# Kernel tuning notes

Hardware: AMD Instinct MI355X
Metric: run time of the kernel (lower is better)

Reference implementation:

```python
import jax, jax.numpy as jnp
import numpy as np

B, T, H, V = 16, 128, 512, 50257


def setup_inputs() -> dict:
    key = jax.random.key(0)
    ks = jax.random.split(key, 6)
    s = 0.05  # init_scale
    return {
        "tokens": jax.random.randint(ks[0], (B, T), 0, V, dtype=jnp.int32),
        "labels": jax.random.randint(ks[1], (B, T), 0, V, dtype=jnp.int32),
        "embedding": jax.random.normal(ks[2], (V, H), jnp.float32) * s,
        "W1": jax.random.normal(ks[3], (2 * H, 4 * H), jnp.float32) * s,
        "b1": jnp.zeros((4 * H,), jnp.float32),
        "W2": jax.random.normal(ks[4], (2 * H, 4 * H), jnp.float32) * s,
        "b2": jnp.zeros((4 * H,), jnp.float32),
        "softmax_w": jax.random.normal(ks[5], (H, V), jnp.float32) * s,
        "softmax_b": jnp.zeros((V,), jnp.float32),
    }


def _lstm_cell(x, h, c, W, b):
    # TF LSTMCell gate order: i, j (candidate), f, o; forget_bias = 0.0
    z = jnp.concatenate([x, h], axis=-1) @ W + b  # [B, 4H]
    i, j, f, o = jnp.split(z, 4, axis=-1)
    c_new = c * jax.nn.sigmoid(f) + jax.nn.sigmoid(i) * jnp.tanh(j)
    h_new = jnp.tanh(c_new) * jax.nn.sigmoid(o)
    return h_new, c_new


def _forward(tokens, labels, embedding, W1, b1, W2, b2, softmax_w, softmax_b):
    x = embedding[tokens]                 # [B, T, H] embedding lookup
    xs = jnp.swapaxes(x, 0, 1)            # [T, B, H] time-major for scan
    zeros = jnp.zeros((B, H), x.dtype)

    def step(carry, xt):
        c1, h1, c2, h2 = carry
        h1n, c1n = _lstm_cell(xt, h1, c1, W1, b1)
        h2n, c2n = _lstm_cell(h1n, h2, c2, W2, b2)
        return (c1n, h1n, c2n, h2n), h2n

    _, hs = jax.lax.scan(step, (zeros, zeros, zeros, zeros), xs)  # hs: [T, B, H]
    output = jnp.swapaxes(hs, 0, 1).reshape(-1, H)                # [B*T, H]
    logits = output @ softmax_w + softmax_b                       # [B*T, V]
    logp = jax.nn.log_softmax(logits, axis=-1)
    ll = jnp.take_along_axis(logp, labels.reshape(-1, 1), axis=1)[:, 0]
    cost = -jnp.sum(ll) / B  # sequence_loss_by_example summed, / batch_size
    return cost


def reference(tokens, labels, embedding, W1, b1, W2, b2, softmax_w, softmax_b):
    return _forward(tokens, labels, embedding, W1, b1, W2, b2, softmax_w, softmax_b)
```

## Files before the change

kernel.cpp:

```cpp
#include <hip/hip_runtime.h>

#define B_ 16
#define T_ 128
#define H_ 512
#define V_ 50257
#define VP_ 50304
#define NBLK 393
#define M_ (B_*T_)
#define N4H 2048
#define KH 512
#define NKB 16
#define FP_ 32
#define NTILES (NBLK * 16)
#define NWORK 224
#define NCHUNK (VP_ * 16 / 16)
#define HP_ 520

typedef __attribute__((ext_vector_type(8))) short short8;
typedef __attribute__((ext_vector_type(4))) float floatx4;
typedef unsigned long long u64;

static __device__ __forceinline__ unsigned short f2bf(float f) {
    unsigned int u = __builtin_bit_cast(unsigned int, f);
    unsigned int r = (u + 0x7FFFu + ((u >> 16) & 1u)) >> 16;
    return (unsigned short)r;
}
static __device__ __forceinline__ u64 ld_ic(const u64* p) {
    return __hip_atomic_load(p, __ATOMIC_RELAXED, __HIP_MEMORY_SCOPE_AGENT);
}
static __device__ __forceinline__ void st_ic(u64* p, u64 v) {
    __hip_atomic_store(p, v, __ATOMIC_RELAXED, __HIP_MEMORY_SCOPE_AGENT);
}
static __device__ __forceinline__ short8 mk_frag(u64 a, u64 b) {
    union { u64 u[2]; short8 s8; } cv;
    cv.u[0] = a; cv.u[1] = b;
    return cv.s8;
}

__global__ void k_init(const int* __restrict__ labels, int* __restrict__ lab_r,
                       unsigned short* __restrict__ zeroh, int* __restrict__ flags) {
    int tid = blockIdx.x * blockDim.x + threadIdx.x;
    if (tid < M_) {
        int t = tid >> 4, b = tid & 15;
        lab_r[tid] = labels[b * T_ + t];
    }
    if (tid < B_ * H_) zeroh[tid] = 0;
    if (tid < 34 * FP_) flags[tid] = 0;
}

__global__ void k_embed(const int* __restrict__ tokens, const float* __restrict__ emb,
                        unsigned short* __restrict__ X) {
    int tid = blockIdx.x * blockDim.x + threadIdx.x;
    if (tid >= M_ * H_) return;
    int row = tid >> 9, col = tid & 511;
    int t = row >> 4, b = row & 15;
    int tok = tokens[b * T_ + t];
    X[tid] = f2bf(emb[(size_t)tok * H_ + col]);
}

__global__ void k_pack(const float* __restrict__ src, int ld, int nvalid, int nkb,
                       int nchunks, unsigned short* __restrict__ dst) {
    int tid = blockIdx.x * blockDim.x + threadIdx.x;
    int lane = tid & 63, chunk = tid >> 6;
    if (chunk >= nchunks) return;
    int nt = chunk / nkb, kb = chunk % nkb;
    int n = nt * 16 + (lane & 15);
    int k = kb * 32 + ((lane >> 4) << 3);
    unsigned short vals[8];
    if (n < nvalid) {
#pragma unroll
        for (int j = 0; j < 8; ++j) vals[j] = f2bf(src[(size_t)(k + j) * ld + n]);
    } else {
#pragma unroll
        for (int j = 0; j < 8; ++j) vals[j] = 0;
    }
    *(short8*)(dst + (size_t)chunk * 512 + lane * 8) = *(short8*)vals;
}

__global__ __launch_bounds__(256, 2) void k_gemm_bias(
        const unsigned short* __restrict__ A, const unsigned short* __restrict__ Bp,
        const float* __restrict__ bias, float* __restrict__ C) {
    int bn = blockIdx.x, bm = blockIdx.y;
    int tid = threadIdx.x, lane = tid & 63, w = tid >> 6;
    int wm = w >> 1, wn = w & 1;
    int l15 = lane & 15, quad = lane >> 4;
    floatx4 acc[4][4];
#pragma unroll
    for (int i = 0; i < 4; ++i)
#pragma unroll
        for (int j = 0; j < 4; ++j) acc[i][j] = (floatx4){0.f, 0.f, 0.f, 0.f};
    const unsigned short* Abase = A + (size_t)(bm * 128 + wm * 64 + l15) * KH + quad * 8;
    int ntg0 = bn * 8 + wn * 4;
#pragma unroll 4
    for (int kb = 0; kb < NKB; ++kb) {
        short8 af[4], bf[4];
#pragma unroll
        for (int mt = 0; mt < 4; ++mt) af[mt] = *(const short8*)(Abase + mt * 16 * KH + kb * 32);
#pragma unroll
        for (int nt = 0; nt < 4; ++nt)
            bf[nt] = *(const short8*)(Bp + ((size_t)(ntg0 + nt) * NKB + kb) * 512 + lane * 8);
#pragma unroll
        for (int mt = 0; mt < 4; ++mt)
#pragma unroll
            for (int nt = 0; nt < 4; ++nt)
                acc[mt][nt] = __builtin_amdgcn_mfma_f32_16x16x32_bf16(af[mt], bf[nt], acc[mt][nt], 0, 0, 0);
    }
#pragma unroll
    for (int nt = 0; nt < 4; ++nt) {
        int col = bn * 128 + wn * 64 + nt * 16 + l15;
        float bv = bias[col];
#pragma unroll
        for (int mt = 0; mt < 4; ++mt) {
            int row0 = bm * 128 + wm * 64 + mt * 16 + quad * 4;
#pragma unroll
            for (int r = 0; r < 4; ++r)
                C[(size_t)(row0 + r) * N4H + col] = acc[mt][nt][r] + bv;
        }
    }
}

__global__ __launch_bounds__(512, 2) void k_mega(
        const float* __restrict__ Zpre1, const unsigned short* __restrict__ W1hP,
        const unsigned short* __restrict__ W2P, const float* __restrict__ b2,
        const unsigned short* __restrict__ zeroh,
        unsigned short* __restrict__ H1, unsigned short* __restrict__ H2,
        int* __restrict__ flags,
        const float* __restrict__ sw, unsigned short* __restrict__ SWP,
        const float* __restrict__ sb, const int* __restrict__ lab_r,
        float* __restrict__ pm, float* __restrict__ ps, float* __restrict__ labv) {
    const int blk = blockIdx.x, tid = threadIdx.x;
    const int lane = tid & 63, w = tid >> 6;
    const int l15 = lane & 15, quad = lane >> 4;
    __shared__ unsigned short hs1[16 * HP_];
    __shared__ unsigned short hs2[16 * HP_];
    __shared__ float zs[128 * 17];
    u64* H1u = (u64*)H1;
    u64* H2u = (u64*)H2;

    if (blk < 32) {
        const bool isL2 = blk >= 16;
        const int bj = isL2 ? blk - 16 : blk;
        const int g = w >> 1, half = w & 1;
        const int nt = g * 32 + bj * 2 + half;

        short8 bfr[32];
        if (!isL2) {
#pragma unroll
            for (int kb = 0; kb < 16; ++kb)
                bfr[kb] = *(const short8*)(W1hP + (size_t)(nt * 16 + kb) * 512 + lane * 8);
        } else {
#pragma unroll
            for (int kb = 0; kb < 32; ++kb)
                bfr[kb] = *(const short8*)(W2P + (size_t)(nt * 32 + kb) * 512 + lane * 8);
        }
        const float b2c = isL2 ? b2[g * 512 + bj * 32 + half * 16 + l15] : 0.f;
        float creg = 0.f;

        for (int s = 0; s < T_; ++s) {
            if (w == 0 && (s > 0 || isL2)) {
                int tgt = 0x80000000;
                int* fp = flags;
                if (!isL2) {
                    if (lane < 16) { fp = flags + lane * FP_; tgt = s; }
                } else {
                    if (lane < 16) { fp = flags + lane * FP_; tgt = s + 1; }
                    else if (lane < 32) { fp = flags + lane * FP_; tgt = s; }
                }
                bool act = (!isL2 && lane < 16) || (isL2 && lane < 32);
                while (true) {
                    int v = act ? __hip_atomic_load(fp, __ATOMIC_RELAXED, __HIP_MEMORY_SCOPE_AGENT)
                                : 0x7fffffff;
                    if (__all(v >= tgt)) break;
                    __builtin_amdgcn_s_sleep(1);
                }
            }
            __syncthreads();

            if (!isL2) {
                const u64* src = (s == 0) ? (const u64*)zeroh : H1u + (size_t)(s - 1) * 1024;
#pragma unroll
                for (int j = 0; j < 4; ++j) {
                    int idx = j * 512 + tid;
                    u64 v = ld_ic(src + idx);
                    *(u64*)(&hs1[(idx >> 7) * HP_ + (idx & 127) * 4]) = v;
                }
            } else {
                const u64* s1 = H1u + (size_t)s * 1024;
                const u64* s2 = (s == 0) ? (const u64*)zeroh : H2u + (size_t)(s - 1) * 1024;
#pragma unroll
                for (int j = 0; j < 4; ++j) {
                    int idx = j * 512 + tid;
                    u64 v = ld_ic(s1 + idx);
                    *(u64*)(&hs1[(idx >> 7) * HP_ + (idx & 127) * 4]) = v;
                }
#pragma unroll
                for (int j = 0; j < 4; ++j) {
                    int idx = j * 512 + tid;
                    u64 v = ld_ic(s2 + idx);
                    *(u64*)(&hs2[(idx >> 7) * HP_ + (idx & 127) * 4]) = v;
                }
            }
            __syncthreads();

            if (!isL2) {
                floatx4 a0 = (floatx4){0.f,0.f,0.f,0.f}, a1 = (floatx4){0.f,0.f,0.f,0.f};
#pragma unroll
                for (int kb = 0; kb < 8; ++kb) {
                    short8 af = *(const short8*)(&hs1[l15 * HP_ + kb * 32 + quad * 8]);
                    a0 = __builtin_amdgcn_mfma_f32_16x16x32_bf16(af, bfr[kb], a0, 0, 0, 0);
                }
#pragma unroll
                for (int kb = 8; kb < 16; ++kb) {
                    short8 af = *(const short8*)(&hs1[l15 * HP_ + kb * 32 + quad * 8]);
                    a1 = __builtin_amdgcn_mfma_f32_16x16x32_bf16(af, bfr[kb], a1, 0, 0, 0);
                }
                const int colg = g * 512 + bj * 32 + half * 16 + l15;
                const int zcol = g * 32 + half * 16 + l15;
#pragma unroll
                for (int r = 0; r < 4; ++r) {
                    int b = quad * 4 + r;
                    zs[zcol * 17 + b] = a0[r] + a1[r] + Zpre1[(size_t)(s * 16 + b) * N4H + colg];
                }
            } else {
                floatx4 a0 = (floatx4){0.f,0.f,0.f,0.f}, a1 = (floatx4){0.f,0.f,0.f,0.f};
#pragma unroll
                for (int kb = 0; kb < 16; ++kb) {
                    short8 af = *(const short8*)(&hs1[l15 * HP_ + kb * 32 + quad * 8]);
                    a0 = __builtin_amdgcn_mfma_f32_16x16x32_bf16(af, bfr[kb], a0, 0, 0, 0);
                }
#pragma unroll
                for (int kb = 0; kb < 16; ++kb) {
                    short8 af = *(const short8*)(&hs2[l15 * HP_ + kb * 32 + quad * 8]);
                    a1 = __builtin_amdgcn_mfma_f32_16x16x32_bf16(af, bfr[16 + kb], a1, 0, 0, 0);
                }
                const int zcol = g * 32 + half * 16 + l15;
#pragma unroll
                for (int r = 0; r < 4; ++r)
                    zs[zcol * 17 + quad * 4 + r] = a0[r] + a1[r] + b2c;
            }
            __syncthreads();

            {
                int u = tid >> 4, b = tid & 15;
                float zi = zs[(0 * 32 + u) * 17 + b];
                float zj = zs[(1 * 32 + u) * 17 + b];
                float zf = zs[(2 * 32 + u) * 17 + b];
                float zo = zs[(3 * 32 + u) * 17 + b];
                float si = 1.f / (1.f + __expf(-zi));
                float sf = 1.f / (1.f + __expf(-zf));
                float so = 1.f / (1.f + __expf(-zo));
                float cn = creg * sf + si * tanhf(zj);
                creg = cn;
                int hvi = (int)f2bf(tanhf(cn) * so);
                int lb = lane & 15;
                unsigned int h0 = (unsigned int)__shfl(hvi, lb);
                unsigned int h1v = (unsigned int)__shfl(hvi, lb + 16);
                unsigned int h2v = (unsigned int)__shfl(hvi, lb + 32);
                unsigned int h3v = (unsigned int)__shfl(hvi, lb + 48);
                if (lane < 16) {
                    u64 v = (u64)(h0 | (h1v << 16)) | ((u64)(h2v | (h3v << 16)) << 32);
                    u64* Hd = isL2 ? H2u : H1u;
                    st_ic(Hd + (size_t)(s * 16 + lane) * 128 + bj * 8 + w, v);
                }
            }
            __builtin_amdgcn_s_waitcnt(0x0F70);
            __syncthreads();
            if (tid == 0)
                __hip_atomic_store(flags + blk * FP_, s + 1, __ATOMIC_RELAXED,
                                   __HIP_MEMORY_SCOPE_AGENT);
        }
    } else {
        const int wid = blk - 32;
        int* wdone = flags + 32 * FP_;

        for (int t = 0; ; ++t) {
            int c = wid + NWORK * (8 * t + w);
            if (c >= NCHUNK) break;
            int cnt = c >> 4, ckb = c & 15;
            int n = cnt * 16 + l15;
            int kk = ckb * 32 + quad * 8;
            unsigned short vals[8];
            if (n < V_) {
#pragma unroll
                for (int j = 0; j < 8; ++j) vals[j] = f2bf(sw[(size_t)(kk + j) * V_ + n]);
            } else {
#pragma unroll
                for (int j = 0; j < 8; ++j) vals[j] = 0;
            }
            u64 v0 = (u64)vals[0] | ((u64)vals[1] << 16) | ((u64)vals[2] << 32) | ((u64)vals[3] << 48);
            u64 v1 = (u64)vals[4] | ((u64)vals[5] << 16) | ((u64)vals[6] << 32) | ((u64)vals[7] << 48);
            u64* dst = (u64*)(SWP + (size_t)c * 512 + lane * 8);
            st_ic(dst, v0);
            st_ic(dst + 1, v1);
        }
        __builtin_amdgcn_s_waitcnt(0x0F70);
        __syncthreads();
        if (tid == 0)
            __hip_atomic_fetch_add(wdone, 1, __ATOMIC_RELAXED, __HIP_MEMORY_SCOPE_AGENT);
        if (w == 0) {
            while (true) {
                int v = (lane == 0)
                    ? __hip_atomic_load(wdone, __ATOMIC_RELAXED, __HIP_MEMORY_SCOPE_AGENT)
                    : 0x7fffffff;
                if (__all(v >= NWORK)) break;
                __builtin_amdgcn_s_sleep(8);
            }
        }
        __syncthreads();

        int done_seen = 0;
        for (int k = wid; k < NTILES; k += NWORK) {
            int bm = k / NBLK, bn = k - bm * NBLK;
            int tgt = bm * 8 + 8;
            if (tgt > done_seen) {
                if (w == 0) {
                    int* fp = flags + (16 + (lane & 15)) * FP_;
                    while (true) {
                        int v = (lane < 16)
                            ? __hip_atomic_load(fp, __ATOMIC_RELAXED, __HIP_MEMORY_SCOPE_AGENT)
                            : 0x7fffffff;
                        if (__all(v >= tgt)) break;
                        __builtin_amdgcn_s_sleep(8);
                    }
                }
                __syncthreads();
                done_seen = tgt;
            }
            floatx4 acc[8];
#pragma unroll
            for (int j = 0; j < 8; ++j) acc[j] = (floatx4){0.f, 0.f, 0.f, 0.f};
            const u64* Abase = H2u + (size_t)(bm * 128 + w * 16 + l15) * 128 + quad * 2;
            int ntg0 = bn * 8;
#pragma unroll 4
            for (int kb = 0; kb < NKB; ++kb) {
                u64 aa = ld_ic(Abase + kb * 8);
                u64 ab = ld_ic(Abase + kb * 8 + 1);
                short8 af = mk_frag(aa, ab);
#pragma unroll
                for (int nt = 0; nt < 8; ++nt) {
                    short8 bf = *(const short8*)(SWP + ((size_t)(ntg0 + nt) * NKB + kb) * 512 + lane * 8);
                    acc[nt] = __builtin_amdgcn_mfma_f32_16x16x32_bf16(af, bf, acc[nt], 0, 0, 0);
                }
            }
            float bv[8]; int colg[8]; bool valid[8];
#pragma unroll
            for (int nt = 0; nt < 8; ++nt) {
                colg[nt] = bn * 128 + nt * 16 + l15;
                valid[nt] = colg[nt] < V_;
                bv[nt] = valid[nt] ? sb[colg[nt]] : 0.f;
            }
#pragma unroll
            for (int r = 0; r < 4; ++r) {
                float m = -3.0e38f;
#pragma unroll
                for (int nt = 0; nt < 8; ++nt) {
                    float v = valid[nt] ? acc[nt][r] + bv[nt] : -3.0e38f;
                    acc[nt][r] = v;
                    m = fmaxf(m, v);
                }
#pragma unroll
                for (int d = 1; d < 16; d <<= 1) m = fmaxf(m, __shfl_xor(m, d, 16));
                float sm = 0.f;
#pragma unroll
                for (int nt = 0; nt < 8; ++nt)
                    if (valid[nt]) sm += __expf(acc[nt][r] - m);
#pragma unroll
                for (int d = 1; d < 16; d <<= 1) sm += __shfl_xor(sm, d, 16);
                int rowg = bm * 128 + w * 16 + quad * 4 + r;
                int lc = lab_r[rowg];
#pragma unroll
                for (int nt = 0; nt < 8; ++nt)
                    if (valid[nt] && colg[nt] == lc) labv[rowg] = acc[nt][r];
                if (l15 == 0) {
                    pm[(size_t)rowg * NBLK + bn] = m;
                    ps[(size_t)rowg * NBLK + bn] = sm;
                }
            }
        }
    }
}

__global__ void k_rowreduce(const float* __restrict__ pm, const float* __restrict__ ps,
                            const float* __restrict__ labv, float* __restrict__ ll) {
    int row = blockIdx.x;
    int lane = threadIdx.x;
    const float* pmr = pm + (size_t)row * NBLK;
    const float* psr = ps + (size_t)row * NBLK;
    float m = -3.0e38f;
    for (int j = lane; j < NBLK; j += 64) m = fmaxf(m, pmr[j]);
#pragma unroll
    for (int d = 1; d < 64; d <<= 1) m = fmaxf(m, __shfl_xor(m, d, 64));
    float s = 0.f;
    for (int j = lane; j < NBLK; j += 64) s += psr[j] * __expf(pmr[j] - m);
#pragma unroll
    for (int d = 1; d < 64; d <<= 1) s += __shfl_xor(s, d, 64);
    if (lane == 0) ll[row] = labv[row] - m - logf(s);
}

__global__ void k_final(const float* __restrict__ ll, float* __restrict__ out) {
    int lane = threadIdx.x;
    float s = 0.f;
    for (int i = lane; i < M_; i += 64) s += ll[i];
#pragma unroll
    for (int d = 1; d < 64; d <<= 1) s += __shfl_xor(s, d, 64);
    if (lane == 0) out[0] = -s / (float)B_;
}

extern "C" void kernel_launch(void* const* d_in, const int* in_sizes, int n_in,
                              void* d_out, int out_size, void* d_ws, size_t ws_size,
                              hipStream_t stream) {
    const int* tokens = (const int*)d_in[0];
    const int* labels = (const int*)d_in[1];
    const float* emb = (const float*)d_in[2];
    const float* W1 = (const float*)d_in[3];
    const float* b1 = (const float*)d_in[4];
    const float* W2 = (const float*)d_in[5];
    const float* b2 = (const float*)d_in[6];
    const float* sw = (const float*)d_in[7];
    const float* sb = (const float*)d_in[8];
    float* out = (float*)d_out;

    char* ws = (char*)d_ws;
    size_t off = 0;
    auto alloc = [&](size_t bytes) {
        void* p = ws + off;
        off = (off + bytes + 255) & ~(size_t)255;
        return p;
    };
    unsigned short* X    = (unsigned short*)alloc((size_t)M_ * KH * 2);
    unsigned short* H1   = (unsigned short*)alloc((size_t)M_ * KH * 2);
    unsigned short* H2   = (unsigned short*)alloc((size_t)M_ * KH * 2);
    unsigned short* W1xP = (unsigned short*)alloc((size_t)N4H * KH * 2);
    unsigned short* W1hP = (unsigned short*)alloc((size_t)N4H * KH * 2);
    unsigned short* W2P  = (unsigned short*)alloc((size_t)N4H * KH * 2 * 2);
    unsigned short* SWP  = (unsigned short*)alloc((size_t)VP_ * KH * 2);
    float* Z     = (float*)alloc((size_t)M_ * N4H * 4);
    unsigned short* zeroh = (unsigned short*)alloc((size_t)B_ * H_ * 2);
    float* pm   = (float*)alloc((size_t)M_ * NBLK * 4);
    float* ps   = (float*)alloc((size_t)M_ * NBLK * 4);
    float* labv = (float*)alloc((size_t)M_ * 4);
    int*   lab_r = (int*)alloc((size_t)M_ * 4);
    float* ll   = (float*)alloc((size_t)M_ * 4);
    int*   flags = (int*)alloc((size_t)34 * FP_ * 4);

    k_init<<<64, 256, 0, stream>>>(labels, lab_r, zeroh, flags);
    k_embed<<<(M_ * H_) / 256, 256, 0, stream>>>(tokens, emb, X);
    k_pack<<<512, 256, 0, stream>>>(W1,                      N4H, N4H, 16, 2048, W1xP);
    k_pack<<<512, 256, 0, stream>>>(W1 + (size_t)512 * N4H,  N4H, N4H, 16, 2048, W1hP);
    k_pack<<<1024, 256, 0, stream>>>(W2,                     N4H, N4H, 32, 4096, W2P);

    k_gemm_bias<<<dim3(16, 16), 256, 0, stream>>>(X, W1xP, b1, Z);

    k_mega<<<256, 512, 0, stream>>>(Z, W1hP, W2P, b2, zeroh, H1, H2, flags,
                                    sw, SWP, sb, lab_r, pm, ps, labv);

    k_rowreduce<<<M_, 64, 0, stream>>>(pm, ps, labv, ll);
    k_final<<<1, 64, 0, stream>>>(ll, out);
}
```

Before: 864.7 us.

## Fuse recurrent weight packing into mega kernel and widen hidden-state loads

Drops the two k_pack launches for the recurrent W1 and W2 slices. The recurrent blocks now read the fp32 weights directly and convert them to bf16 register fragments at kernel start. The relaxed 8-byte atomic loads of H1/H2 become plain 16-byte vector loads, both in the recurrent staging and in the softmax GEMM. Zpre1 is also prefetched before the flag wait, which takes global latency off the serial step. The risks are slow strided fp32 loads during the one-time weight conversion, and possible stale cached reads of cross-block data now that the atomic loads are gone.

```diff
diff --git a/kernel.cpp b/kernel.cpp
--- a/kernel.cpp
+++ b/kernel.cpp
@@ -25,16 +25,8 @@
     unsigned int r = (u + 0x7FFFu + ((u >> 16) & 1u)) >> 16;
     return (unsigned short)r;
 }
-static __device__ __forceinline__ u64 ld_ic(const u64* p) {
-    return __hip_atomic_load(p, __ATOMIC_RELAXED, __HIP_MEMORY_SCOPE_AGENT);
-}
 static __device__ __forceinline__ void st_ic(u64* p, u64 v) {
     __hip_atomic_store(p, v, __ATOMIC_RELAXED, __HIP_MEMORY_SCOPE_AGENT);
-}
-static __device__ __forceinline__ short8 mk_frag(u64 a, u64 b) {
-    union { u64 u[2]; short8 s8; } cv;
-    cv.u[0] = a; cv.u[1] = b;
-    return cv.s8;
 }
 
 __global__ void k_init(const int* __restrict__ labels, int* __restrict__ lab_r,
@@ -120,8 +112,8 @@
 }
 
 __global__ __launch_bounds__(512, 2) void k_mega(
-        const float* __restrict__ Zpre1, const unsigned short* __restrict__ W1hP,
-        const unsigned short* __restrict__ W2P, const float* __restrict__ b2,
+        const float* __restrict__ Zpre1, const float* __restrict__ W1,
+        const float* __restrict__ W2, const float* __restrict__ b2,
         const unsigned short* __restrict__ zeroh,
         unsigned short* __restrict__ H1, unsigned short* __restrict__ H2,
         int* __restrict__ flags,
@@ -142,21 +134,39 @@
         const int bj = isL2 ? blk - 16 : blk;
         const int g = w >> 1, half = w & 1;
         const int nt = g * 32 + bj * 2 + half;
+        const int colg = g * 512 + bj * 32 + half * 16 + l15;
 
         short8 bfr[32];
-        if (!isL2) {
-#pragma unroll
-            for (int kb = 0; kb < 16; ++kb)
-                bfr[kb] = *(const short8*)(W1hP + (size_t)(nt * 16 + kb) * 512 + lane * 8);
-        } else {
-#pragma unroll
-            for (int kb = 0; kb < 32; ++kb)
-                bfr[kb] = *(const short8*)(W2P + (size_t)(nt * 32 + kb) * 512 + lane * 8);
-        }
-        const float b2c = isL2 ? b2[g * 512 + bj * 32 + half * 16 + l15] : 0.f;
+        {
+            unsigned short vals[8];
+            if (!isL2) {
+#pragma unroll
+                for (int kb = 0; kb < 16; ++kb) {
+#pragma unroll
+                    for (int j = 0; j < 8; ++j)
+                        vals[j] = f2bf(W1[(size_t)(512 + kb * 32 + quad * 8 + j) * N4H + nt * 16 + l15]);
+                    bfr[kb] = *(short8*)vals;
+                }
+            } else {
+#pragma unroll
+                for (int kb = 0; kb < 32; ++kb) {
+#pragma unroll
+                    for (int j = 0; j < 8; ++j)
+                        vals[j] = f2bf(W2[(size_t)(kb * 32 + quad * 8 + j) * N4H + nt * 16 + l15]);
+                    bfr[kb] = *(short8*)vals;
+                }
+            }
+        }
+        const float b2c = isL2 ? b2[colg] : 0.f;
         float creg = 0.f;
 
         for (int s = 0; s < T_; ++s) {
+            float zpre[4];
+            if (!isL2) {
+#pragma unroll
+                for (int r = 0; r < 4; ++r)
+                    zpre[r] = Zpre1[(size_t)(s * 16 + quad * 4 + r) * N4H + colg];
+            }
             if (w == 0 && (s > 0 || isL2)) {
                 int tgt = 0x80000000;
                 int* fp = flags;
@@ -177,27 +187,29 @@
             __syncthreads();
 
             if (!isL2) {
-                const u64* src = (s == 0) ? (const u64*)zeroh : H1u + (size_t)(s - 1) * 1024;
-#pragma unroll
-                for (int j = 0; j < 4; ++j) {
+                const short8* src = (const short8*)((s == 0) ? zeroh
+                                       : H1 + (size_t)(s - 1) * B_ * H_);
+#pragma unroll
+                for (int j = 0; j < 2; ++j) {
                     int idx = j * 512 + tid;
-                    u64 v = ld_ic(src + idx);
-                    *(u64*)(&hs1[(idx >> 7) * HP_ + (idx & 127) * 4]) = v;
+                    short8 v = src[idx];
+                    *(short8*)(&hs1[(idx >> 6) * HP_ + (idx & 63) * 8]) = v;
                 }
             } else {
-                const u64* s1 = H1u + (size_t)s * 1024;
-                const u64* s2 = (s == 0) ? (const u64*)zeroh : H2u + (size_t)(s - 1) * 1024;
-#pragma unroll
-                for (int j = 0; j < 4; ++j) {
+                const short8* s1 = (const short8*)(H1 + (size_t)s * B_ * H_);
+                const short8* s2 = (const short8*)((s == 0) ? zeroh
+                                       : H2 + (size_t)(s - 1) * B_ * H_);
+#pragma unroll
+                for (int j = 0; j < 2; ++j) {
                     int idx = j * 512 + tid;
-                    u64 v = ld_ic(s1 + idx);
-                    *(u64*)(&hs1[(idx >> 7) * HP_ + (idx & 127) * 4]) = v;
-                }
-#pragma unroll
-                for (int j = 0; j < 4; ++j) {
+                    short8 v = s1[idx];
+                    *(short8*)(&hs1[(idx >> 6) * HP_ + (idx & 63) * 8]) = v;
+                }
+#pragma unroll
+                for (int j = 0; j < 2; ++j) {
                     int idx = j * 512 + tid;
-                    u64 v = ld_ic(s2 + idx);
-                    *(u64*)(&hs2[(idx >> 7) * HP_ + (idx & 127) * 4]) = v;
+                    short8 v = s2[idx];
+                    *(short8*)(&hs2[(idx >> 6) * HP_ + (idx & 63) * 8]) = v;
                 }
             }
             __syncthreads();
@@ -214,13 +226,10 @@
                     short8 af = *(const short8*)(&hs1[l15 * HP_ + kb * 32 + quad * 8]);
                     a1 = __builtin_amdgcn_mfma_f32_16x16x32_bf16(af, bfr[kb], a1, 0, 0, 0);
                 }
-                const int colg = g * 512 + bj * 32 + half * 16 + l15;
                 const int zcol = g * 32 + half * 16 + l15;
 #pragma unroll
-                for (int r = 0; r < 4; ++r) {
-                    int b = quad * 4 + r;
-                    zs[zcol * 17 + b] = a0[r] + a1[r] + Zpre1[(size_t)(s * 16 + b) * N4H + colg];
-                }
+                for (int r = 0; r < 4; ++r)
+                    zs[zcol * 17 + quad * 4 + r] = a0[r] + a1[r] + zpre[r];
             } else {
                 floatx4 a0 = (floatx4){0.f,0.f,0.f,0.f}, a1 = (floatx4){0.f,0.f,0.f,0.f};
 #pragma unroll
@@ -329,13 +338,11 @@
             floatx4 acc[8];
 #pragma unroll
             for (int j = 0; j < 8; ++j) acc[j] = (floatx4){0.f, 0.f, 0.f, 0.f};
-            const u64* Abase = H2u + (size_t)(bm * 128 + w * 16 + l15) * 128 + quad * 2;
+            const short8* Abase = (const short8*)(H2 + (size_t)(bm * 128 + w * 16 + l15) * KH) + quad;
             int ntg0 = bn * 8;
 #pragma unroll 4
             for (int kb = 0; kb < NKB; ++kb) {
-                u64 aa = ld_ic(Abase + kb * 8);
-                u64 ab = ld_ic(Abase + kb * 8 + 1);
-                short8 af = mk_frag(aa, ab);
+                short8 af = Abase[kb * 4];
 #pragma unroll
                 for (int nt = 0; nt < 8; ++nt) {
                     short8 bf = *(const short8*)(SWP + ((size_t)(ntg0 + nt) * NKB + kb) * 512 + lane * 8);
@@ -431,8 +438,6 @@
     unsigned short* H1   = (unsigned short*)alloc((size_t)M_ * KH * 2);
     unsigned short* H2   = (unsigned short*)alloc((size_t)M_ * KH * 2);
     unsigned short* W1xP = (unsigned short*)alloc((size_t)N4H * KH * 2);
-    unsigned short* W1hP = (unsigned short*)alloc((size_t)N4H * KH * 2);
-    unsigned short* W2P  = (unsigned short*)alloc((size_t)N4H * KH * 2 * 2);
     unsigned short* SWP  = (unsigned short*)alloc((size_t)VP_ * KH * 2);
     float* Z     = (float*)alloc((size_t)M_ * N4H * 4);
     unsigned short* zeroh = (unsigned short*)alloc((size_t)B_ * H_ * 2);
@@ -445,13 +450,11 @@
 
     k_init<<<64, 256, 0, stream>>>(labels, lab_r, zeroh, flags);
     k_embed<<<(M_ * H_) / 256, 256, 0, stream>>>(tokens, emb, X);
-    k_pack<<<512, 256, 0, stream>>>(W1,                      N4H, N4H, 16, 2048, W1xP);
-    k_pack<<<512, 256, 0, stream>>>(W1 + (size_t)512 * N4H,  N4H, N4H, 16, 2048, W1hP);
-    k_pack<<<1024, 256, 0, stream>>>(W2,                     N4H, N4H, 32, 4096, W2P);
+    k_pack<<<512, 256, 0, stream>>>(W1, N4H, N4H, 16, 2048, W1xP);
 
     k_gemm_bias<<<dim3(16, 16), 256, 0, stream>>>(X, W1xP, b1, Z);
 
-    k_mega<<<256, 512, 0, stream>>>(Z, W1hP, W2P, b2, zeroh, H1, H2, flags,
+    k_mega<<<256, 512, 0, stream>>>(Z, W1, W2, b2, zeroh, H1, H2, flags,
                                     sw, SWP, sb, lab_r, pm, ps, labv);
 
     k_rowreduce<<<M_, 64, 0, stream>>>(pm, ps, labv, ll);
```

Measured after the change: 765.0 us. -11.5%, faster.
